# Kernel optimization log

Measured on AMD Instinct MI355X. Metric: run time of the kernel, lower is better.

Reference implementation:

```python
import jax, jax.numpy as jnp
import numpy as np

B, S, D, H = 2, 2048, 1024, 16
DK = D // H

def setup_inputs() -> dict:
    key = jax.random.key(0)
    ks = jax.random.split(key, 8)
    def lin(k):
        kw, kb = jax.random.split(k)
        w = jax.random.normal(kw, (D, D), dtype=jnp.float32) / np.sqrt(D)
        b = jax.random.normal(kb, (D,), dtype=jnp.float32) * 0.01
        return w, b
    wq, bq = lin(ks[0]); wk, bk = lin(ks[1]); wv, bv = lin(ks[2]); wo, bo = lin(ks[3])
    return {
        'q': jax.random.normal(ks[4], (B, S, D), dtype=jnp.float32),
        'k': jax.random.normal(ks[5], (B, S, D), dtype=jnp.float32),
        'v': jax.random.normal(ks[6], (B, S, D), dtype=jnp.float32),
        'mask': jnp.ones((1, 1, S, S), dtype=jnp.int32),
        'wq': wq, 'bq': bq, 'wk': wk, 'bk': bk,
        'wv': wv, 'bv': bv, 'wo': wo, 'bo': bo,
    }

def reference(q, k, v, mask, wq, bq, wk, bk, wv, bv, wo, bo):
    b, s, _ = q.shape
    # QKV projections (nn.Linear: x @ W^T + b)
    Q = (q @ wq.T + bq).reshape(b, s, H, DK).transpose(0, 2, 1, 3)  # [B,H,S,DK]
    K = (k @ wk.T + bk).reshape(b, -1, H, DK).transpose(0, 2, 1, 3)
    V = (v @ wv.T + bv).reshape(b, -1, H, DK).transpose(0, 2, 1, 3)
    scores = jnp.einsum('bhqd,bhkd->bhqk', Q, K) / np.sqrt(DK)
    # faithful to source: masked positions set to -1e-09 (tiny, as written)
    scores = jnp.where(mask == 0, jnp.float32(-1e-09), scores)
    att = jax.nn.softmax(scores, axis=-1)
    x = jnp.einsum('bhqk,bhkd->bhqd', att, V)
    x = x.transpose(0, 2, 1, 3).reshape(b, s, H * DK)
    return x @ wo.T + bo
```

## Files before the change

### kernel.cpp

```cpp
#include <hip/hip_runtime.h>
#include <stdint.h>

typedef unsigned short u16;
typedef unsigned int u32;
typedef __bf16 bf16x8 __attribute__((ext_vector_type(8)));
typedef __bf16 bf16x2 __attribute__((ext_vector_type(2)));
typedef float f32x4 __attribute__((ext_vector_type(4)));
typedef float f32x16 __attribute__((ext_vector_type(16)));
typedef unsigned short u16x4 __attribute__((ext_vector_type(4)));
typedef unsigned short u16x8 __attribute__((ext_vector_type(8)));
typedef u32 u32x4 __attribute__((ext_vector_type(4)));

#define B_ 2
#define S_ 2048
#define D_ 1024
#define H_ 16

__device__ __forceinline__ u16 f2bf(float f) {
  uint32_t u = __builtin_bit_cast(uint32_t, f);
  u += 0x7FFF + ((u >> 16) & 1);
  return (u16)(u >> 16);
}

__device__ __forceinline__ u32 pkbf(float x, float y) {
  bf16x2 t;
  t.x = (__bf16)x;
  t.y = (__bf16)y;
  return __builtin_bit_cast(u32, t);
}

__device__ __forceinline__ void pl32swap(u32& a, u32& b) {
  asm("v_permlane32_swap_b32 %0, %1" : "+v"(a), "+v"(b));
}

__device__ __forceinline__ void gld_lds16(const void* g, void* l) {
  __builtin_amdgcn_global_load_lds((const __attribute__((address_space(1))) void*)g,
                                   (__attribute__((address_space(3))) void*)l, 16, 0, 0);
}

__global__ void cvt_all(const float* __restrict__ q, const float* __restrict__ k,
                        const float* __restrict__ v, const float* __restrict__ wq,
                        const float* __restrict__ wk, const float* __restrict__ wv,
                        const float* __restrict__ wo, u16* __restrict__ qb,
                        u16* __restrict__ kb, u16* __restrict__ vb, u16* __restrict__ wqb,
                        u16* __restrict__ wkb, u16* __restrict__ wvb, u16* __restrict__ wob) {
  int bid = blockIdx.x;
  const float* s;
  u16* d;
  int base;
  if (bid < 4096)       { s = q;  d = qb;  base = bid; }
  else if (bid < 8192)  { s = k;  d = kb;  base = bid - 4096; }
  else if (bid < 12288) { s = v;  d = vb;  base = bid - 8192; }
  else if (bid < 13312) { s = wq; d = wqb; base = bid - 12288; }
  else if (bid < 14336) { s = wk; d = wkb; base = bid - 13312; }
  else if (bid < 15360) { s = wv; d = wvb; base = bid - 14336; }
  else                  { s = wo; d = wob; base = bid - 15360; }
  int i = (base * 256 + threadIdx.x) * 4;
  float4 f = *(const float4*)(s + i);
  u16x4 o;
  o.x = f2bf(f.x); o.y = f2bf(f.y); o.z = f2bf(f.z); o.w = f2bf(f.w);
  *(u16x4*)(d + i) = o;
}

template <int EPI, int BN>
__device__ __forceinline__ void gemm_body(const u16* __restrict__ A, const u16* __restrict__ W,
                                          const float* __restrict__ bias, void* __restrict__ Cp,
                                          float scale, int m0, int n0) {
  constexpr int K = 1024;
  constexpr int N = 1024;
  constexpr int NFR = BN / 32;
  __shared__ __align__(16) u16 As[128 * 64];
  __shared__ __align__(16) u16 Ws[BN * 64];
  const int tid = threadIdx.x;
  const int lane = tid & 63, wid = tid >> 6;
  const int wm = wid >> 1, wn = wid & 1;
  const int l15 = lane & 15, l4 = lane >> 4;

  f32x4 acc[4][NFR] = {};

  for (int kt = 0; kt < K / 64; ++kt) {
    __syncthreads();
#pragma unroll
    for (int i = 0; i < 4; ++i) {
      int c = i * 256 + tid;
      int row = c >> 3;
      int scb = ((c & 7) << 4) ^ ((row & 7) << 4);
      size_t goff = (size_t)kt * 64 + (scb >> 1);
      gld_lds16(A + (size_t)(m0 + row) * K + goff, (char*)As + (size_t)c * 16);
    }
#pragma unroll
    for (int i = 0; i < BN / 32; ++i) {
      int c = i * 256 + tid;
      int row = c >> 3;
      int scb = ((c & 7) << 4) ^ ((row & 7) << 4);
      gld_lds16(W + (size_t)(n0 + row) * K + (size_t)kt * 64 + (scb >> 1),
                (char*)Ws + (size_t)c * 16);
    }
    __syncthreads();
#pragma unroll
    for (int kk = 0; kk < 2; ++kk) {
      bf16x8 af[4], bfr[NFR];
#pragma unroll
      for (int m = 0; m < 4; ++m) {
        int row = wm * 64 + m * 16 + l15;
        int cb = (kk * 64 + l4 * 16) ^ ((row & 7) << 4);
        af[m] = *(const bf16x8*)((const char*)As + row * 128 + cb);
      }
#pragma unroll
      for (int n = 0; n < NFR; ++n) {
        int row = wn * (BN / 2) + n * 16 + l15;
        int cb = (kk * 64 + l4 * 16) ^ ((row & 7) << 4);
        bfr[n] = *(const bf16x8*)((const char*)Ws + row * 128 + cb);
      }
#pragma unroll
      for (int m = 0; m < 4; ++m)
#pragma unroll
        for (int n = 0; n < NFR; ++n)
          acc[m][n] = __builtin_amdgcn_mfma_f32_16x16x32_bf16(af[m], bfr[n], acc[m][n], 0, 0, 0);
    }
  }

  if (EPI == 0) {
    float* C = (float*)Cp;
#pragma unroll
    for (int m = 0; m < 4; ++m)
#pragma unroll
      for (int n = 0; n < NFR; ++n) {
        int col = n0 + wn * (BN / 2) + n * 16 + l15;
        float bval = bias[col];
#pragma unroll
        for (int j = 0; j < 4; ++j) {
          int r = m0 + wm * 64 + m * 16 + l4 * 4 + j;
          C[(size_t)r * N + col] = acc[m][n][j] + bval;
        }
      }
  } else if (EPI == 1) {
    u16* C = (u16*)Cp;
#pragma unroll
    for (int m = 0; m < 4; ++m)
#pragma unroll
      for (int n = 0; n < NFR; ++n) {
        int col = n0 + wn * (BN / 2) + n * 16 + l15;
        float bval = bias[col];
        int h = col >> 6, dk = col & 63;
#pragma unroll
        for (int j = 0; j < 4; ++j) {
          int r = m0 + wm * 64 + m * 16 + l4 * 4 + j;
          int bb = r >> 11, s = r & 2047;
          C[(((size_t)bb * H_ + h) * S_ + s) * 64 + dk] = f2bf((acc[m][n][j] + bval) * scale);
        }
      }
  } else {
    u16* C = (u16*)Cp;
#pragma unroll
    for (int m = 0; m < 4; ++m)
#pragma unroll
      for (int n = 0; n < NFR; ++n) {
        int col = n0 + wn * (BN / 2) + n * 16 + l15;
        float bval = bias[col];
        int h = col >> 6, dk = col & 63;
        int r0 = m0 + wm * 64 + m * 16 + l4 * 4;
        int bb = r0 >> 11, s0 = r0 & 2047;
        u16x4 o;
#pragma unroll
        for (int j = 0; j < 4; ++j) o[j] = f2bf(acc[m][n][j] + bval);
        *(u16x4*)(C + (((size_t)bb * H_ + h) * 64 + dk) * S_ + s0) = o;
      }
  }
}

__global__ __launch_bounds__(256) void gemm_qkv(
    const u16* __restrict__ qb, const u16* __restrict__ kb, const u16* __restrict__ vb,
    const u16* __restrict__ wqb, const u16* __restrict__ wkb, const u16* __restrict__ wvb,
    const float* __restrict__ bq, const float* __restrict__ bk, const float* __restrict__ bv,
    u16* __restrict__ Qp, u16* __restrict__ Kp, u16* __restrict__ VTp) {
  const int flat = blockIdx.x;
  const int nf = (flat & 7) * 96 + (flat >> 3);
  const int zz = nf >> 8, rem = nf & 255;
  const int n0 = (rem & 7) * 128, m0 = (rem >> 3) * 128;
  if (zz == 2) {
    gemm_body<2, 128>(vb, wvb, bv, VTp, 1.0f, m0, n0);
  } else if (zz == 1) {
    gemm_body<1, 128>(kb, wkb, bk, Kp, 1.0f, m0, n0);
  } else {
    gemm_body<1, 128>(qb, wqb, bq, Qp, 0.1803368801111244f, m0, n0);
  }
}

__global__ __launch_bounds__(256) void gemm_out(
    const u16* __restrict__ xb, const u16* __restrict__ wob,
    const float* __restrict__ bo, float* __restrict__ out) {
  const int flat = blockIdx.x;
  const int nf = (flat & 7) * 64 + (flat >> 3);
  const int n0 = (nf & 15) * 64, m0 = (nf >> 4) * 128;
  gemm_body<0, 64>(xb, wob, bo, out, 1.0f, m0, n0);
}

__global__ __launch_bounds__(256, 2) void attn(
    const u16* __restrict__ Qp, const u16* __restrict__ Kp,
    const u16* __restrict__ VTp, u16* __restrict__ xb) {
  const int flat = blockIdx.x;
  const int nf = (flat & 7) * 64 + (flat >> 3);
  const int bh = nf >> 4, qt = nf & 15;
  const int b = bh >> 4, h = bh & 15;
  const size_t kbase = (size_t)bh * S_ * 64;
  const int tid = threadIdx.x, lane = tid & 63, w = tid >> 6;
  const int l31 = lane & 31, hi = lane >> 5;

  __shared__ __align__(16) u16 Ks[2][64 * 64];
  __shared__ __align__(16) u16 Vs[2][64 * 64];

  bf16x8 qf[4];
  {
    const u16* qrow = Qp + kbase + (size_t)(qt * 128 + w * 32 + l31) * 64;
#pragma unroll
    for (int kk = 0; kk < 4; ++kk)
      qf[kk] = *(const bf16x8*)(qrow + kk * 16 + hi * 8);
  }

  float m = -1e30f, lsum = 0.f;
  f32x16 xacc[2] = {};

  auto stage = [&](int bi, int t) {
#pragma unroll
    for (int i = 0; i < 2; ++i) {
      int c = i * 256 + tid;
      int row = c >> 3;
      int scb = (((c & 7) ^ (row & 7) ^ ((row >> 3) & 3)) << 4);
      gld_lds16(Kp + kbase + (size_t)(t * 64 + row) * 64 + (scb >> 1),
                (char*)Ks[bi] + (size_t)c * 16);
    }
#pragma unroll
    for (int i = 0; i < 2; ++i) {
      int c = i * 256 + tid;
      int row = c >> 3;
      int scb = (((c & 7) ^ (row & 7) ^ ((row >> 3) & 3)) << 4);
      gld_lds16(VTp + kbase + (size_t)row * S_ + t * 64 + (scb >> 1),
                (char*)Vs[bi] + (size_t)c * 16);
    }
  };

  stage(0, 0);
  for (int t = 0; t < S_ / 64; ++t) {
    const int cur = t & 1;
    __syncthreads();
    if (t + 1 < S_ / 64) stage(cur ^ 1, t + 1);

    const u16* Kb = Ks[cur];
    const u16* Vb = Vs[cur];

    f32x16 sacc[2] = {};
    __builtin_amdgcn_s_setprio(1);
#pragma unroll
    for (int kk = 0; kk < 4; ++kk)
#pragma unroll
      for (int kvt = 0; kvt < 2; ++kvt) {
        int row = kvt * 32 + l31;
        int cb = (kk * 32 + hi * 16) ^ ((((row & 7) ^ ((row >> 3) & 3))) << 4);
        bf16x8 kf = *(const bf16x8*)((const char*)Kb + row * 128 + cb);
        sacc[kvt] = __builtin_amdgcn_mfma_f32_32x32x16_bf16(kf, qf[kk], sacc[kvt], 0, 0, 0);
      }
    __builtin_amdgcn_s_setprio(0);

    float mx;
    {
      float a = fmaxf(fmaxf(sacc[0][0], sacc[0][1]), fmaxf(sacc[0][2], sacc[0][3]));
      float b2 = fmaxf(fmaxf(sacc[0][4], sacc[0][5]), fmaxf(sacc[0][6], sacc[0][7]));
      float c = fmaxf(fmaxf(sacc[0][8], sacc[0][9]), fmaxf(sacc[0][10], sacc[0][11]));
      float d = fmaxf(fmaxf(sacc[0][12], sacc[0][13]), fmaxf(sacc[0][14], sacc[0][15]));
      float e = fmaxf(fmaxf(sacc[1][0], sacc[1][1]), fmaxf(sacc[1][2], sacc[1][3]));
      float f = fmaxf(fmaxf(sacc[1][4], sacc[1][5]), fmaxf(sacc[1][6], sacc[1][7]));
      float g = fmaxf(fmaxf(sacc[1][8], sacc[1][9]), fmaxf(sacc[1][10], sacc[1][11]));
      float h2 = fmaxf(fmaxf(sacc[1][12], sacc[1][13]), fmaxf(sacc[1][14], sacc[1][15]));
      float x = fmaxf(fmaxf(a, b2), fmaxf(c, d));
      float y = fmaxf(fmaxf(e, f), fmaxf(g, h2));
      x = fmaxf(x, y);
      mx = fmaxf(x, __shfl_xor(x, 32, 64));
    }

    if (__any(mx - m > 8.f)) {
      float nm = fmaxf(m, mx);
      float sc = __builtin_amdgcn_exp2f(m - nm);
      m = nm;
      lsum *= sc;
#pragma unroll
      for (int r = 0; r < 16; ++r) {
        int src = ((r & 3) + 8 * (r >> 2) + 4 * hi) | (hi << 5);
        float f = __shfl(sc, src, 64);
        xacc[0][r] *= f;
        xacc[1][r] *= f;
      }
    }

    float p[2][16];
    float sum = 0.f;
#pragma unroll
    for (int t2 = 0; t2 < 2; ++t2)
#pragma unroll
      for (int r = 0; r < 16; ++r) {
        float e = __builtin_amdgcn_exp2f(sacc[t2][r] - m);
        p[t2][r] = e;
        sum += e;
      }
    sum += __shfl_xor(sum, 32, 64);
    lsum += sum;

#pragma unroll
    for (int kk = 0; kk < 4; ++kk) {
      const int t2 = kk >> 1, rb = (kk & 1) * 8;
      u32 a0 = pkbf(p[t2][rb + 0], p[t2][rb + 1]);
      u32 a1 = pkbf(p[t2][rb + 2], p[t2][rb + 3]);
      u32 b0 = pkbf(p[t2][rb + 4], p[t2][rb + 5]);
      u32 b1 = pkbf(p[t2][rb + 6], p[t2][rb + 7]);
      pl32swap(a0, b0);
      pl32swap(a1, b1);
      u32x4 wv;
      wv.x = a0; wv.y = a1; wv.z = b0; wv.w = b1;
      bf16x8 pf = __builtin_bit_cast(bf16x8, wv);
      __builtin_amdgcn_s_setprio(1);
#pragma unroll
      for (int dn = 0; dn < 2; ++dn) {
        int row = dn * 32 + l31;
        int cb = (kk * 32 + hi * 16) ^ ((((row & 7) ^ ((row >> 3) & 3))) << 4);
        bf16x8 vf = *(const bf16x8*)((const char*)Vb + row * 128 + cb);
        xacc[dn] = __builtin_amdgcn_mfma_f32_32x32x16_bf16(pf, vf, xacc[dn], 0, 0, 0);
      }
      __builtin_amdgcn_s_setprio(0);
    }
  }

  float linv = 1.f / lsum;
#pragma unroll
  for (int r = 0; r < 16; ++r) {
    int qr = (r & 3) + 8 * (r >> 2) + 4 * hi;
    float f = __shfl(linv, qr | (hi << 5), 64);
    int qg = qt * 128 + w * 32 + qr;
    size_t rowb = ((size_t)b * S_ + qg) * D_ + h * 64;
    xb[rowb + l31] = f2bf(xacc[0][r] * f);
    xb[rowb + 32 + l31] = f2bf(xacc[1][r] * f);
  }
}

extern "C" void kernel_launch(void* const* d_in, const int* in_sizes, int n_in,
                              void* d_out, int out_size, void* d_ws, size_t ws_size,
                              hipStream_t stream) {
  const float* q  = (const float*)d_in[0];
  const float* k  = (const float*)d_in[1];
  const float* v  = (const float*)d_in[2];
  const float* wq = (const float*)d_in[4];
  const float* bq = (const float*)d_in[5];
  const float* wk = (const float*)d_in[6];
  const float* bk = (const float*)d_in[7];
  const float* wv = (const float*)d_in[8];
  const float* bv = (const float*)d_in[9];
  const float* wo = (const float*)d_in[10];
  const float* bo = (const float*)d_in[11];
  float* out = (float*)d_out;

  char* ws = (char*)d_ws;
  const size_t MB = 1u << 20;
  u16* qb  = (u16*)(ws + 0 * MB);
  u16* kb  = (u16*)(ws + 8 * MB);
  u16* vb  = (u16*)(ws + 16 * MB);
  u16* wqb = (u16*)(ws + 24 * MB);
  u16* wkb = (u16*)(ws + 26 * MB);
  u16* wvb = (u16*)(ws + 28 * MB);
  u16* wob = (u16*)(ws + 30 * MB);
  u16* Qp  = (u16*)(ws + 32 * MB);
  u16* Kp  = (u16*)(ws + 40 * MB);
  u16* VTp = (u16*)(ws + 48 * MB);
  u16* xb  = (u16*)(ws + 56 * MB);

  cvt_all<<<16384, 256, 0, stream>>>(q, k, v, wq, wk, wv, wo,
                                     qb, kb, vb, wqb, wkb, wvb, wob);
  gemm_qkv<<<768, 256, 0, stream>>>(qb, kb, vb, wqb, wkb, wvb,
                                    bq, bk, bv, Qp, Kp, VTp);
  attn<<<512, 256, 0, stream>>>(Qp, Kp, VTp, xb);
  gemm_out<<<512, 256, 0, stream>>>(xb, wob, bo, out);
}
```

Before: 133.7 us.

## Split attention over two KV halves with a separate merge kernel

The attention kernel now processes only half of the key/value sequence per block, doubling the grid. Each block writes a normalized partial output plus its row max and sum. A new merge kernel combines the two halves with log-sum-exp weights into the final layout. The row-max reduction also switches to three-input max chains. This adds a kernel launch, extra global traffic for the partial outputs, and rounding of the partials to bf16.

```diff
diff --git a/kernel.cpp b/kernel.cpp
--- a/kernel.cpp
+++ b/kernel.cpp
@@ -22,6 +22,11 @@
   return (u16)(u >> 16);
 }
 
+__device__ __forceinline__ float bf2f(u16 x) {
+  u32 u = ((u32)x) << 16;
+  return __builtin_bit_cast(float, u);
+}
+
 __device__ __forceinline__ u32 pkbf(float x, float y) {
   bf16x2 t;
   t.x = (__bf16)x;
@@ -31,6 +36,10 @@
 
 __device__ __forceinline__ void pl32swap(u32& a, u32& b) {
   asm("v_permlane32_swap_b32 %0, %1" : "+v"(a), "+v"(b));
+}
+
+__device__ __forceinline__ float max3f(float a, float b, float c) {
+  return fmaxf(fmaxf(a, b), c);
 }
 
 __device__ __forceinline__ void gld_lds16(const void* g, void* l) {
@@ -196,16 +205,16 @@
   gemm_body<0, 64>(xb, wob, bo, out, 1.0f, m0, n0);
 }
 
-__global__ __launch_bounds__(256, 2) void attn(
+__global__ __launch_bounds__(256, 2) void attn_part(
     const u16* __restrict__ Qp, const u16* __restrict__ Kp,
-    const u16* __restrict__ VTp, u16* __restrict__ xb) {
+    const u16* __restrict__ VTp, u16* __restrict__ Op, float2* __restrict__ stats) {
   const int flat = blockIdx.x;
-  const int nf = (flat & 7) * 64 + (flat >> 3);
-  const int bh = nf >> 4, qt = nf & 15;
-  const int b = bh >> 4, h = bh & 15;
+  const int nf = (flat & 7) * 128 + (flat >> 3);
+  const int bh = nf >> 5, half = (nf >> 4) & 1, qt = nf & 15;
   const size_t kbase = (size_t)bh * S_ * 64;
   const int tid = threadIdx.x, lane = tid & 63, w = tid >> 6;
   const int l31 = lane & 31, hi = lane >> 5;
+  const int t0 = half * 16;
 
   __shared__ __align__(16) u16 Ks[2][64 * 64];
   __shared__ __align__(16) u16 Vs[2][64 * 64];
@@ -240,11 +249,11 @@
     }
   };
 
-  stage(0, 0);
-  for (int t = 0; t < S_ / 64; ++t) {
-    const int cur = t & 1;
+  stage(0, t0);
+  for (int tt = 0; tt < 16; ++tt) {
+    const int cur = tt & 1;
     __syncthreads();
-    if (t + 1 < S_ / 64) stage(cur ^ 1, t + 1);
+    if (tt + 1 < 16) stage(cur ^ 1, t0 + tt + 1);
 
     const u16* Kb = Ks[cur];
     const u16* Vb = Vs[cur];
@@ -264,17 +273,22 @@
 
     float mx;
     {
-      float a = fmaxf(fmaxf(sacc[0][0], sacc[0][1]), fmaxf(sacc[0][2], sacc[0][3]));
-      float b2 = fmaxf(fmaxf(sacc[0][4], sacc[0][5]), fmaxf(sacc[0][6], sacc[0][7]));
-      float c = fmaxf(fmaxf(sacc[0][8], sacc[0][9]), fmaxf(sacc[0][10], sacc[0][11]));
-      float d = fmaxf(fmaxf(sacc[0][12], sacc[0][13]), fmaxf(sacc[0][14], sacc[0][15]));
-      float e = fmaxf(fmaxf(sacc[1][0], sacc[1][1]), fmaxf(sacc[1][2], sacc[1][3]));
-      float f = fmaxf(fmaxf(sacc[1][4], sacc[1][5]), fmaxf(sacc[1][6], sacc[1][7]));
-      float g = fmaxf(fmaxf(sacc[1][8], sacc[1][9]), fmaxf(sacc[1][10], sacc[1][11]));
-      float h2 = fmaxf(fmaxf(sacc[1][12], sacc[1][13]), fmaxf(sacc[1][14], sacc[1][15]));
-      float x = fmaxf(fmaxf(a, b2), fmaxf(c, d));
-      float y = fmaxf(fmaxf(e, f), fmaxf(g, h2));
-      x = fmaxf(x, y);
+      float t0_ = max3f(sacc[0][0], sacc[0][1], sacc[0][2]);
+      float t1_ = max3f(sacc[0][3], sacc[0][4], sacc[0][5]);
+      float t2_ = max3f(sacc[0][6], sacc[0][7], sacc[0][8]);
+      float t3_ = max3f(sacc[0][9], sacc[0][10], sacc[0][11]);
+      float t4_ = max3f(sacc[0][12], sacc[0][13], sacc[0][14]);
+      float t5_ = max3f(sacc[0][15], sacc[1][0], sacc[1][1]);
+      float t6_ = max3f(sacc[1][2], sacc[1][3], sacc[1][4]);
+      float t7_ = max3f(sacc[1][5], sacc[1][6], sacc[1][7]);
+      float t8_ = max3f(sacc[1][8], sacc[1][9], sacc[1][10]);
+      float t9_ = max3f(sacc[1][11], sacc[1][12], sacc[1][13]);
+      float ta_ = fmaxf(sacc[1][14], sacc[1][15]);
+      float u0 = max3f(t0_, t1_, t2_);
+      float u1 = max3f(t3_, t4_, t5_);
+      float u2 = max3f(t6_, t7_, t8_);
+      float u3 = fmaxf(t9_, ta_);
+      float x = fmaxf(max3f(u0, u1, u2), u3);
       mx = fmaxf(x, __shfl_xor(x, 32, 64));
     }
 
@@ -330,15 +344,46 @@
   }
 
   float linv = 1.f / lsum;
+  const size_t obase = ((size_t)(half * 32 + bh)) * (S_ * 64);
 #pragma unroll
   for (int r = 0; r < 16; ++r) {
     int qr = (r & 3) + 8 * (r >> 2) + 4 * hi;
     float f = __shfl(linv, qr | (hi << 5), 64);
     int qg = qt * 128 + w * 32 + qr;
-    size_t rowb = ((size_t)b * S_ + qg) * D_ + h * 64;
-    xb[rowb + l31] = f2bf(xacc[0][r] * f);
-    xb[rowb + 32 + l31] = f2bf(xacc[1][r] * f);
-  }
+    Op[obase + (size_t)qg * 64 + l31] = f2bf(xacc[0][r] * f);
+    Op[obase + (size_t)qg * 64 + 32 + l31] = f2bf(xacc[1][r] * f);
+  }
+  if (hi == 0) {
+    int qg = qt * 128 + w * 32 + l31;
+    float2 st;
+    st.x = m;
+    st.y = lsum;
+    stats[(size_t)(half * 32 + bh) * S_ + qg] = st;
+  }
+}
+
+__global__ __launch_bounds__(256) void attn_merge(
+    const u16* __restrict__ Op, const float2* __restrict__ stats,
+    u16* __restrict__ xb) {
+  int gid = blockIdx.x * 256 + threadIdx.x;
+  int row = gid >> 3, seg = gid & 7;
+  int bh = row >> 11, s = row & 2047;
+  int b = bh >> 4, h = bh & 15;
+  float2 st0 = stats[(size_t)bh * S_ + s];
+  float2 st1 = stats[(size_t)(32 + bh) * S_ + s];
+  float mm = fmaxf(st0.x, st1.x);
+  float w0 = st0.y * __builtin_amdgcn_exp2f(st0.x - mm);
+  float w1 = st1.y * __builtin_amdgcn_exp2f(st1.x - mm);
+  float inv = 1.f / (w0 + w1);
+  float c0 = w0 * inv, c1 = w1 * inv;
+  const size_t o0 = (size_t)bh * (S_ * 64) + (size_t)s * 64 + seg * 8;
+  u16x8 a = *(const u16x8*)(Op + o0);
+  u16x8 bb = *(const u16x8*)(Op + (size_t)32 * S_ * 64 + o0);
+  u16x8 o;
+#pragma unroll
+  for (int j = 0; j < 8; ++j)
+    o[j] = f2bf(c0 * bf2f(a[j]) + c1 * bf2f(bb[j]));
+  *(u16x8*)(xb + ((size_t)(b * S_ + s)) * D_ + h * 64 + seg * 8) = o;
 }
 
 extern "C" void kernel_launch(void* const* d_in, const int* in_sizes, int n_in,
@@ -370,11 +415,14 @@
   u16* Kp  = (u16*)(ws + 40 * MB);
   u16* VTp = (u16*)(ws + 48 * MB);
   u16* xb  = (u16*)(ws + 56 * MB);
+  u16* Op     = (u16*)(ws + 0 * MB);
+  float2* st  = (float2*)(ws + 18 * MB);
 
   cvt_all<<<16384, 256, 0, stream>>>(q, k, v, wq, wk, wv, wo,
                                      qb, kb, vb, wqb, wkb, wvb, wob);
   gemm_qkv<<<768, 256, 0, stream>>>(qb, kb, vb, wqb, wkb, wvb,
                                     bq, bk, bv, Qp, Kp, VTp);
-  attn<<<512, 256, 0, stream>>>(Qp, Kp, VTp, xb);
+  attn_part<<<1024, 256, 0, stream>>>(Qp, Kp, VTp, Op, st);
+  attn_merge<<<2048, 256, 0, stream>>>(Op, st, xb);
   gemm_out<<<512, 256, 0, stream>>>(xb, wob, bo, out);
 }
```

After: 137.0 us. 2.5% more time.
